# Performance work log

Hardware: AMD Instinct MI355X
Metric: run time of the kernel (lower is better)

## Reference

```python
import jax, jax.numpy as jnp
import numpy as np

N = 50000      # nodes
E = 800000     # edges (before self-loops)
IN_DIM = 128
HID = 64
OUT = 32
HEADS = 8
BN_EPS = 1e-5
NEG_SLOPE = 0.2  # PyG GATConv default


def setup_inputs() -> dict:
    key = jax.random.key(0)
    ks = jax.random.split(key, 24)
    g = lambda k, shape, fan_in: (jax.random.normal(k, shape, jnp.float32) / np.sqrt(fan_in))
    return {
        "x": jax.random.normal(ks[0], (N, IN_DIM), jnp.float32),
        "edge_index": jax.random.randint(ks[1], (2, E), 0, N, dtype=jnp.int64),
        # GCN1
        "gcn1_w": g(ks[2], (IN_DIM, HID), IN_DIM),
        "gcn1_b": jnp.zeros((HID,), jnp.float32),
        # BN1 (eval mode running stats)
        "bn1_gamma": jnp.ones((HID,), jnp.float32),
        "bn1_beta": jnp.zeros((HID,), jnp.float32),
        "bn1_mean": 0.1 * jax.random.normal(ks[3], (HID,), jnp.float32),
        "bn1_var": 0.5 + jax.random.uniform(ks[4], (HID,), jnp.float32),
        # GAT1: heads=8, per-head out=HID, concat=False -> mean over heads
        "gat1_w": g(ks[5], (HID, HEADS * HID), HID),
        "gat1_asrc": g(ks[6], (HEADS, HID), HID),
        "gat1_adst": g(ks[7], (HEADS, HID), HID),
        "gat1_b": jnp.zeros((HID,), jnp.float32),
        # GCN2
        "gcn2_w": g(ks[8], (HID, HID), HID),
        "gcn2_b": jnp.zeros((HID,), jnp.float32),
        # BN2
        "bn2_gamma": jnp.ones((HID,), jnp.float32),
        "bn2_beta": jnp.zeros((HID,), jnp.float32),
        "bn2_mean": 0.1 * jax.random.normal(ks[9], (HID,), jnp.float32),
        "bn2_var": 0.5 + jax.random.uniform(ks[10], (HID,), jnp.float32),
        # GAT2: heads=8, per-head out=OUT, concat=False
        "gat2_w": g(ks[11], (HID, HEADS * OUT), HID),
        "gat2_asrc": g(ks[12], (HEADS, OUT), OUT),
        "gat2_adst": g(ks[13], (HEADS, OUT), OUT),
        "gat2_b": jnp.zeros((OUT,), jnp.float32),
    }


def _gcn(x, src, dst, w, b, n):
    # PyG GCNConv: x @ W, symmetric norm with self-loops (src/dst already include them)
    h = x @ w
    deg = jax.ops.segment_sum(jnp.ones(src.shape[0], x.dtype), dst, num_segments=n)
    dinv = jnp.where(deg > 0, jax.lax.rsqrt(jnp.maximum(deg, 1.0)), 0.0)
    coef = dinv[src] * dinv[dst]                     # [E']
    out = jax.ops.segment_sum(coef[:, None] * h[src], dst, num_segments=n)
    return out + b


def _gat(x, src, dst, w, a_src, a_dst, b, n, heads, ch):
    # PyG GATConv (concat=False): mean over heads, softmax over incoming edges per dst
    h = (x @ w).reshape(n, heads, ch)                # [N,H,C]
    es = jnp.einsum('nhc,hc->nh', h, a_src)          # alpha_src per node
    ed = jnp.einsum('nhc,hc->nh', h, a_dst)
    e = jax.nn.leaky_relu(es[src] + ed[dst], NEG_SLOPE)  # [E',H]
    m = jax.ops.segment_max(e, dst, num_segments=n)
    m = jnp.where(jnp.isfinite(m), m, 0.0)
    ex = jnp.exp(e - m[dst])
    denom = jax.ops.segment_sum(ex, dst, num_segments=n)
    alpha = ex / (denom[dst] + 1e-16)                # [E',H]
    out = jnp.zeros((n, ch), x.dtype)
    for hd in range(heads):  # fixed small head loop keeps peak edge memory at [E',C]
        msg = alpha[:, hd, None] * h[src, hd]        # [E',C]
        out = out + jax.ops.segment_sum(msg, dst, num_segments=n)
    return out / heads + b


def _bn_eval(x, gamma, beta, mean, var):
    return (x - mean) * jax.lax.rsqrt(var + BN_EPS) * gamma + beta


def reference(x, edge_index,
              gcn1_w, gcn1_b, bn1_gamma, bn1_beta, bn1_mean, bn1_var,
              gat1_w, gat1_asrc, gat1_adst, gat1_b,
              gcn2_w, gcn2_b, bn2_gamma, bn2_beta, bn2_mean, bn2_var,
              gat2_w, gat2_asrc, gat2_adst, gat2_b):
    n = x.shape[0]
    loops = jnp.arange(n, dtype=edge_index.dtype)
    src = jnp.concatenate([edge_index[0], loops])    # self-loops (PyG default)
    dst = jnp.concatenate([edge_index[1], loops])

    h = _gcn(x, src, dst, gcn1_w, gcn1_b, n)
    h = jax.nn.relu(_bn_eval(h, bn1_gamma, bn1_beta, bn1_mean, bn1_var))
    h = jax.nn.relu(_gat(h, src, dst, gat1_w, gat1_asrc, gat1_adst, gat1_b, n, HEADS, HID))
    h = _gcn(h, src, dst, gcn2_w, gcn2_b, n)
    h = jax.nn.relu(_bn_eval(h, bn2_gamma, bn2_beta, bn2_mean, bn2_var))
    h = _gat(h, src, dst, gat2_w, gat2_asrc, gat2_adst, gat2_b, n, HEADS, OUT)
    return jax.nn.log_softmax(h, axis=1)
```

## Files before the change

kernel.cpp:

```cpp
#include <hip/hip_runtime.h>
#include <hip/hip_bf16.h>

#define NN 50000
#define NE 800000
#define IND 128
#define NH 8
#define EBLK 256
#define EPB 3125
#define NBUK 391
#define NBUKP 392
#define GH (NBUKP * EBLK)
#define PREPB 308

typedef __hip_bfloat16 bf16;
typedef __attribute__((ext_vector_type(8))) short short8;
typedef __attribute__((ext_vector_type(8))) __bf16 bf16x8;
typedef __attribute__((ext_vector_type(4))) float floatx4;
typedef __attribute__((ext_vector_type(2))) float floatx2;

static __device__ __forceinline__ short f2bf_bits(float f) {
    unsigned u = __float_as_uint(f);
    u = (u + 0x7fffu + ((u >> 16) & 1u)) >> 16;
    return (short)u;
}
static __device__ __forceinline__ float bf2f(bf16 v) { return __bfloat162float(v); }
static __device__ __forceinline__ floatx2 up2(unsigned av) {
    floatx2 r;
    r.x = __uint_as_float(av << 16);
    r.y = __uint_as_float(av & 0xffff0000u);
    return r;
}
static __device__ __forceinline__ unsigned pk2(float a, float b) {
    return (unsigned)(unsigned short)f2bf_bits(a) | ((unsigned)(unsigned short)f2bf_bits(b) << 16);
}
static __device__ __forceinline__ void pk_fma_lo(floatx2& acc, floatx2 a, floatx2 al) {
    asm("v_pk_fma_f32 %0, %1, %2, %0 op_sel:[0,0,0] op_sel_hi:[1,0,1]"
        : "+v"(acc) : "v"(a), "v"(al));
}
static __device__ __forceinline__ void pk_fma_hi(floatx2& acc, floatx2 a, floatx2 al) {
    asm("v_pk_fma_f32 %0, %1, %2, %0 op_sel:[0,1,0] op_sel_hi:[1,1,1]"
        : "+v"(acc) : "v"(a), "v"(al));
}

static __device__ __forceinline__ void scan_buckets(const int* __restrict__ bsum,
        int* sp, int* gb, int tid) {
    int v0 = (2 * tid < NBUKP) ? bsum[2 * tid] : 0;
    int v1 = (2 * tid + 1 < NBUKP) ? bsum[2 * tid + 1] : 0;
    int c = v0 + v1;
    sp[tid] = c; __syncthreads();
    int val = c;
#pragma unroll
    for (int off = 1; off < 256; off <<= 1) {
        int t = (tid >= off) ? sp[tid - off] : 0;
        __syncthreads();
        val += t; sp[tid] = val;
        __syncthreads();
    }
    int pex = val - c;
    gb[2 * tid] = pex;
    gb[2 * tid + 1] = pex + v0;
    __syncthreads();
}

__global__ __launch_bounds__(256) void bin_count_prep_kernel(const int* __restrict__ edst,
        int* __restrict__ ghist,
        const float* __restrict__ gcn1_w, const float* __restrict__ gcn2_w,
        const float* __restrict__ gat1_w, const float* __restrict__ gat2_w,
        const float* __restrict__ as1, const float* __restrict__ ad1,
        const float* __restrict__ as2, const float* __restrict__ ad2,
        bf16* __restrict__ wT1, bf16* __restrict__ wT2,
        bf16* __restrict__ wgT1, bf16* __restrict__ wgT2,
        float* __restrict__ was1, float* __restrict__ wad1,
        float* __restrict__ was2, float* __restrict__ wad2) {
    __shared__ int hsh[NBUKP];
    const int tid = threadIdx.x;
    if (blockIdx.x < EBLK) {
        const int blk = blockIdx.x;
        for (int b = tid; b < NBUKP; b += 256) hsh[b] = 0;
        __syncthreads();
        const int e0 = blk * EPB;
        for (int e = e0 + tid; e < e0 + EPB; e += 256)
            atomicAdd(&hsh[edst[e] >> 7], 1);
        __syncthreads();
        for (int b = tid; b < NBUKP; b += 256)
            ghist[b * EBLK + blk] = hsh[b];
    } else {
        int idx = (blockIdx.x - EBLK) * 256 + tid;
        if (idx < 8192) {
            int m = idx >> 7, k = idx & 127;
            ((short*)wT1)[idx] = f2bf_bits(gcn1_w[(long)k * 64 + m]);
        } else if (idx < 12288) {
            int i = idx - 8192;
            int m = i >> 6, k = i & 63;
            ((short*)wT2)[i] = f2bf_bits(gcn2_w[(long)k * 64 + m]);
        } else if (idx < 45056) {
            int i = idx - 12288;
            int m = i >> 9, k = i & 511;
            int h = k >> 6, c = k & 63;
            ((short*)wgT1)[i] = f2bf_bits(gat1_w[(long)c * 512 + h * 64 + m]);
        } else if (idx < 77824) {
            int i = idx - 45056;
            int m = i >> 9, k = i & 511;
            int h = k >> 6, c = k & 63;
            ((short*)wgT2)[i] = (m < 32) ? f2bf_bits(gat2_w[(long)c * 256 + h * 32 + m]) : (short)0;
        } else if (idx < 78336) {
            int i = idx - 77824;
            int h = i >> 6, c = i & 63;
            const float* wrow = gat1_w + (long)c * 512 + h * 64;
            float s = 0.f, d = 0.f;
            for (int cc = 0; cc < 64; ++cc) {
                float w = wrow[cc];
                s += w * as1[h * 64 + cc];
                d += w * ad1[h * 64 + cc];
            }
            was1[i] = s; wad1[i] = d;
        } else if (idx < 78848) {
            int i = idx - 78336;
            int h = i >> 6, c = i & 63;
            const float* wrow = gat2_w + (long)c * 256 + h * 32;
            float s = 0.f, d = 0.f;
            for (int cc = 0; cc < 32; ++cc) {
                float w = wrow[cc];
                s += w * as2[h * 32 + cc];
                d += w * ad2[h * 32 + cc];
            }
            was2[i] = s; wad2[i] = d;
        }
    }
}

__global__ __launch_bounds__(256) void scang1_kernel(const int* __restrict__ src,
        int* __restrict__ pre, int* __restrict__ bsum, int n) {
    __shared__ int sh[256];
    const int tid = threadIdx.x;
    const int idx = blockIdx.x * 256 + tid;
    int c = (idx < n) ? src[idx] : 0;
    sh[tid] = c; __syncthreads();
    int val = c;
#pragma unroll
    for (int off = 1; off < 256; off <<= 1) {
        int t = (tid >= off) ? sh[tid - off] : 0;
        __syncthreads();
        val += t; sh[tid] = val;
        __syncthreads();
    }
    if (idx < n) pre[idx] = val - c;
    if (tid == 255) bsum[blockIdx.x] = val;
}

__global__ __launch_bounds__(256) void bin_scatter_kernel(const int* __restrict__ esrc,
        const int* __restrict__ edst, const int* __restrict__ gpre,
        const int* __restrict__ bsum, unsigned* __restrict__ ebuf) {
    __shared__ int cur[NBUKP];
    __shared__ int sp[256], gb[512];
    const int tid = threadIdx.x, blk = blockIdx.x;
    scan_buckets(bsum, sp, gb, tid);
    for (int b = tid; b < NBUKP; b += 256)
        cur[b] = gpre[b * EBLK + blk] + gb[b];
    __syncthreads();
    const int e0 = blk * EPB;
    for (int e = e0 + tid; e < e0 + EPB; e += 256) {
        int d = edst[e], s = esrc[e];
        int pos = atomicAdd(&cur[d >> 7], 1);
        ebuf[pos] = ((unsigned)(d & 127) << 16) | (unsigned)s;
    }
}

__global__ __launch_bounds__(256) void bucket_finalize_kernel(const unsigned* __restrict__ ebuf,
        const int* __restrict__ gpre, const int* __restrict__ bsum,
        int* __restrict__ rowptr, float* __restrict__ dinv, int* __restrict__ csrc) {
    __shared__ int lh[128], lcur[128], sc[256];
    __shared__ int sp[256], gb[512];
    const int bu = blockIdx.x, tid = threadIdx.x;
    scan_buckets(bsum, sp, gb, tid);
    const int seg_beg = gpre[bu * EBLK] + gb[bu];
    const int seg_end = gpre[(bu + 1) * EBLK] + gb[bu + 1];
    if (tid < 128) lh[tid] = 0;
    __syncthreads();
    for (int i = seg_beg + tid; i < seg_end; i += 256)
        atomicAdd(&lh[ebuf[i] >> 16], 1);
    __syncthreads();
    int c = (tid < 128) ? lh[tid] : 0;
    sc[tid] = c; __syncthreads();
    int val = c;
#pragma unroll
    for (int off = 1; off < 256; off <<= 1) {
        int t = (tid >= off) ? sc[tid - off] : 0;
        __syncthreads();
        val += t; sc[tid] = val;
        __syncthreads();
    }
    int excl = val - c;
    if (tid < 128) {
        lcur[tid] = excl;
        int node = bu * 128 + tid;
        if (node < NN) {
            rowptr[node] = seg_beg + excl;
            dinv[node] = rsqrtf((float)c + 1.f);
        }
    }
    if (bu == 0 && tid == 0) rowptr[NN] = NE;
    __syncthreads();
    for (int i = seg_beg + tid; i < seg_end; i += 256) {
        unsigned u = ebuf[i];
        int pos = atomicAdd(&lcur[u >> 16], 1);
        csrc[seg_beg + pos] = (int)(u & 0xffffu);
    }
}

template<int K, int EPI, bool AF32>
__global__ __launch_bounds__(256) void mm2_kernel(const void* __restrict__ A,
        const bf16* __restrict__ wT, void* __restrict__ C,
        const float* __restrict__ bias, const float* __restrict__ rowscale,
        int nrows, int M) {
    const int row0 = blockIdx.x * 64;
    const int tid = threadIdx.x;
    const int lane = tid & 63, wave = tid >> 6;
    const int lr = lane & 15, q = lane >> 4;
    const int row = row0 + wave * 16 + lr;
    const bool rok = row < nrows;
    constexpr int NC = (EPI == 4) ? 2 : 4;
    floatx4 acc[NC] = {};
#pragma unroll 4
    for (int k0 = 0; k0 < K; k0 += 32) {
        short8 av = {0, 0, 0, 0, 0, 0, 0, 0};
        if (rok) {
            if (AF32) {
                const float* apf = (const float*)A + (long)row * K + q * 8 + k0;
                floatx4 va = *(const floatx4*)apf;
                floatx4 vb = *(const floatx4*)(apf + 4);
#pragma unroll
                for (int j = 0; j < 4; ++j) { av[j] = f2bf_bits(va[j]); av[4 + j] = f2bf_bits(vb[j]); }
            } else {
                av = *(const short8*)((const short*)A + (long)row * K + q * 8 + k0);
            }
        }
        bf16x8 a = __builtin_bit_cast(bf16x8, av);
#pragma unroll
        for (int c = 0; c < NC; ++c) {
            bf16x8 b = __builtin_bit_cast(bf16x8,
                *(const short8*)((const short*)wT + (long)(c * 16 + lr) * K + k0 + q * 8));
            acc[c] = __builtin_amdgcn_mfma_f32_16x16x32_bf16(a, b, acc[c], 0, 0, 0);
        }
    }
    if (EPI == 4) {
#pragma unroll
        for (int r = 0; r < 4; ++r) {
            int orow = row0 + wave * 16 + q * 4 + r;
            float v0 = acc[0][r] * 0.125f + bias[lr];
            float v1 = acc[1][r] * 0.125f + bias[16 + lr];
            float m = fmaxf(v0, v1);
#pragma unroll
            for (int off = 1; off < 16; off <<= 1) m = fmaxf(m, __shfl_xor(m, off));
            float s = __expf(v0 - m) + __expf(v1 - m);
#pragma unroll
            for (int off = 1; off < 16; off <<= 1) s += __shfl_xor(s, off);
            float ls = m + logf(s);
            if (orow < nrows) {
                ((float*)C)[(long)orow * 32 + lr] = v0 - ls;
                ((float*)C)[(long)orow * 32 + 16 + lr] = v1 - ls;
            }
        }
        return;
    }
#pragma unroll
    for (int c = 0; c < NC; ++c)
#pragma unroll
        for (int r = 0; r < 4; ++r) {
            int orow = row0 + wave * 16 + q * 4 + r;
            int col = c * 16 + lr;
            if (orow < nrows && col < M) {
                long o = (long)orow * M + col;
                float v = acc[c][r];
                if (EPI == 0) ((float*)C)[o] = v;
                else if (EPI == 2) {
                    v = v * 0.125f + bias[col];
                    ((bf16*)C)[o] = __float2bfloat16(fmaxf(v, 0.f));
                } else {
                    ((bf16*)C)[o] = __float2bfloat16(rowscale[orow] * v);
                }
            }
        }
}

__global__ __launch_bounds__(256) void gcn_fused_kernel(const int* __restrict__ rowptr,
        const int* __restrict__ csrc, const float* __restrict__ dinv,
        const bf16* __restrict__ hin, const float* __restrict__ b,
        const float* __restrict__ gamma, const float* __restrict__ beta,
        const float* __restrict__ mean, const float* __restrict__ var,
        bf16* __restrict__ actout) {
    const int node = blockIdx.x * 4 + (threadIdx.x >> 6);
    if (node >= NN) return;
    const int lane = threadIdx.x & 63;
    const int eslot = lane >> 5, cp = lane & 31;
    const unsigned cpo = 4u * (unsigned)cp;
    const int beg = __builtin_amdgcn_readfirstlane(rowptr[node]);
    const int end = __builtin_amdgcn_readfirstlane(rowptr[node + 1]);
    const float di = dinv[node];
    const int* csp = csrc + beg;
    floatx2 acc2 = {0.f, 0.f};
    const int dn = end - beg;
    const int kup = (dn + 15) & ~15;
    for (int k0 = 0; k0 < kup; k0 += 16) {
        int s_[8]; float w_[8];
#pragma unroll
        for (int u = 0; u < 8; ++u) {
            int k = k0 + 2 * u + eslot;
            int ok = k < dn;
            s_[u] = csp[ok ? k : 0];
            w_[u] = ok ? 1.f : 0.f;
        }
        unsigned av_[8];
#pragma unroll
        for (int u = 0; u < 8; ++u)
            av_[u] = *(const unsigned*)((const char*)hin + ((unsigned)s_[u] * 128u + cpo));
#pragma unroll
        for (int u = 0; u < 8; ++u) {
            floatx2 a2 = up2(av_[u]);
            acc2 += a2 * w_[u];
        }
    }
    acc2.x += __shfl_xor(acc2.x, 32);
    acc2.y += __shfl_xor(acc2.y, 32);
    {
        unsigned sv = *(const unsigned*)((const char*)hin + ((unsigned)node * 128u + cpo));
        acc2 += up2(sv);
    }
    int c0 = 2 * cp, c1 = c0 + 1;
    float x0 = acc2.x * di + b[c0];
    float x1 = acc2.y * di + b[c1];
    x0 = (x0 - mean[c0]) * rsqrtf(var[c0] + 1e-5f) * gamma[c0] + beta[c0];
    x1 = (x1 - mean[c1]) * rsqrtf(var[c1] + 1e-5f) * gamma[c1] + beta[c1];
    if (eslot == 0)
        *(unsigned*)((unsigned short*)actout + (long)node * 64 + c0) =
            pk2(fmaxf(x0, 0.f), fmaxf(x1, 0.f));
}

__global__ __launch_bounds__(256) void scores_kernel(const bf16* __restrict__ actb,
        const float* __restrict__ was, const float* __restrict__ wad,
        float* __restrict__ es, float* __restrict__ ed, int n) {
    const int node = blockIdx.x * 4 + (threadIdx.x >> 6);
    if (node >= n) return;
    const int lane = threadIdx.x & 63;
    const int h = lane >> 3, cg = lane & 7;
    short8 a8 = *(const short8*)((const short*)actb + (long)node * 64 + cg * 8);
    const float* wsp = was + h * 64 + cg * 8;
    const float* wdp = wad + h * 64 + cg * 8;
    floatx4 ws0 = *(const floatx4*)wsp, ws1 = *(const floatx4*)(wsp + 4);
    floatx4 wd0 = *(const floatx4*)wdp, wd1 = *(const floatx4*)(wdp + 4);
    float s = 0.f, d = 0.f;
#pragma unroll
    for (int j = 0; j < 4; ++j) {
        float v0 = bf2f(__builtin_bit_cast(bf16, a8[j]));
        float v1 = bf2f(__builtin_bit_cast(bf16, a8[4 + j]));
        s += v0 * ws0[j] + v1 * ws1[j];
        d += v0 * wd0[j] + v1 * wd1[j];
    }
#pragma unroll
    for (int off = 1; off < 8; off <<= 1) {
        s += __shfl_xor(s, off);
        d += __shfl_xor(d, off);
    }
    if (cg == 0) { es[node * NH + h] = s; ed[node * NH + h] = d; }
}

__global__ __launch_bounds__(256) void gat_agg_kernel(const int* __restrict__ rowptr,
        const int* __restrict__ csrc, const float* __restrict__ es, const float* __restrict__ ed,
        const bf16* __restrict__ actb, bf16* __restrict__ agg) {
    __shared__ __align__(16) float salpha[4][512];
    __shared__ int ssrcs[4][64];
    __shared__ __align__(16) float sself[4][8];
    const int wv = threadIdx.x >> 6;
    const int node = blockIdx.x * 4 + wv;
    if (node >= NN) return;
    const int lane = threadIdx.x & 63;
    const int h = lane & 7, slot = lane >> 3;
    const int beg = __builtin_amdgcn_readfirstlane(rowptr[node]);
    const int end = __builtin_amdgcn_readfirstlane(rowptr[node + 1]);
    const int deg = end - beg;
    const int* csp = csrc + beg;
    const float edr = *(const float*)((const char*)ed + ((unsigned)node * 32u + (unsigned)h * 4u));

    float selfe = *(const float*)((const char*)es + ((unsigned)node * 32u + (unsigned)h * 4u)) + edr;
    selfe = selfe > 0.f ? selfe : 0.2f * selfe;

    if (deg <= 64) {
        const int nb = (deg + 7) >> 3;
        const int dm1 = (deg > 0) ? deg - 1 : 0;
        float ex_r[8]; int s_r[8];
        float den = 0.f;
#pragma unroll
        for (int b = 0; b < 8; ++b) { ex_r[b] = 0.f; s_r[b] = 0; }
        if (deg > 0) {
#pragma unroll
            for (int b = 0; b < 8; ++b)
                if (b < nb) {
                    int k = b * 8 + slot;
                    s_r[b] = csp[k < deg ? k : dm1];
                }
#pragma unroll
            for (int b = 0; b < 8; ++b)
                if (b < nb) {
                    float e = *(const float*)((const char*)es +
                              ((unsigned)s_r[b] * 32u + (unsigned)h * 4u)) + edr;
                    e = e > 0.f ? e : 0.2f * e;
                    float ex = __expf(e - selfe);
                    ex_r[b] = (b * 8 + slot < deg) ? ex : 0.f;
                    den += ex_r[b];
                }
        }
        den += __shfl_xor(den, 8);
        den += __shfl_xor(den, 16);
        den += __shfl_xor(den, 32);
        const float invden = 1.f / (den + 1.f);

#pragma unroll
        for (int b = 0; b < 8; ++b)
            if (b < nb) salpha[wv][b * 64 + lane] = ex_r[b] * invden;
        if (h == 0) {
#pragma unroll
            for (int b = 0; b < 8; ++b)
                if (b < nb) ssrcs[wv][b * 8 + slot] = s_r[b];
        }
        if (slot == 0) sself[wv][h] = invden;

        const int hq = lane >> 5, cp = lane & 31;
        const unsigned cpo = 4u * (unsigned)cp;
        floatx2 acc2[4] = {};
        const int ng = nb;
        if (ng > 0) {
            int sA0, sA1, sA2, sA3, sA4, sA5, sA6, sA7;
            int sB0, sB1, sB2, sB3, sB4, sB5, sB6, sB7;
            unsigned rA0, rA1, rA2, rA3, rA4, rA5, rA6, rA7;
            unsigned rB0, rB1, rB2, rB3, rB4, rB5, rB6, rB7;
#define LOAD_BANK(S, R, G) do { \
    const int* sp_ = &ssrcs[wv][(G) * 8]; \
    S##0 = sp_[0]; S##1 = sp_[1]; S##2 = sp_[2]; S##3 = sp_[3]; \
    S##4 = sp_[4]; S##5 = sp_[5]; S##6 = sp_[6]; S##7 = sp_[7]; \
    R##0 = *(const unsigned*)((const char*)actb + ((unsigned)S##0 * 128u + cpo)); \
    R##1 = *(const unsigned*)((const char*)actb + ((unsigned)S##1 * 128u + cpo)); \
    R##2 = *(const unsigned*)((const char*)actb + ((unsigned)S##2 * 128u + cpo)); \
    R##3 = *(const unsigned*)((const char*)actb + ((unsigned)S##3 * 128u + cpo)); \
    R##4 = *(const unsigned*)((const char*)actb + ((unsigned)S##4 * 128u + cpo)); \
    R##5 = *(const unsigned*)((const char*)actb + ((unsigned)S##5 * 128u + cpo)); \
    R##6 = *(const unsigned*)((const char*)actb + ((unsigned)S##6 * 128u + cpo)); \
    R##7 = *(const unsigned*)((const char*)actb + ((unsigned)S##7 * 128u + cpo)); \
} while (0)
#define FMA_BANK(R, G) do { \
    const float* ab_ = &salpha[wv][(G) * 64 + hq * 4]; \
    unsigned rr_[8] = {R##0, R##1, R##2, R##3, R##4, R##5, R##6, R##7}; \
    _Pragma("unroll") \
    for (int j_ = 0; j_ < 8; ++j_) { \
        floatx4 al_ = *(const floatx4*)(ab_ + j_ * 8); \
        floatx2 al01_ = __builtin_shufflevector(al_, al_, 0, 1); \
        floatx2 al23_ = __builtin_shufflevector(al_, al_, 2, 3); \
        floatx2 a2_ = up2(rr_[j_]); \
        pk_fma_lo(acc2[0], a2_, al01_); pk_fma_hi(acc2[1], a2_, al01_); \
        pk_fma_lo(acc2[2], a2_, al23_); pk_fma_hi(acc2[3], a2_, al23_); \
    } \
} while (0)
            LOAD_BANK(sA, rA, 0);
            int g = 0;
            while (true) {
                if (g + 1 < ng) LOAD_BANK(sB, rB, g + 1);
                FMA_BANK(rA, g);
                ++g; if (g >= ng) break;
                if (g + 1 < ng) LOAD_BANK(sA, rA, g + 1);
                FMA_BANK(rB, g);
                ++g; if (g >= ng) break;
            }
#undef LOAD_BANK
#undef FMA_BANK
        }
        {
            unsigned sv = *(const unsigned*)((const char*)actb + ((unsigned)node * 128u + cpo));
            floatx2 a2 = up2(sv);
            floatx4 sa = *(const floatx4*)&sself[wv][hq * 4];
            floatx2 sa01 = __builtin_shufflevector(sa, sa, 0, 1);
            floatx2 sa23 = __builtin_shufflevector(sa, sa, 2, 3);
            pk_fma_lo(acc2[0], a2, sa01); pk_fma_hi(acc2[1], a2, sa01);
            pk_fma_lo(acc2[2], a2, sa23); pk_fma_hi(acc2[3], a2, sa23);
        }
#pragma unroll
        for (int j = 0; j < 4; ++j)
            *(unsigned*)((unsigned short*)agg + (long)node * 512 + (hq * 4 + j) * 64 + 2 * cp) =
                pk2(acc2[j].x, acc2[j].y);
    } else {
        float acc[NH] = {0.f, 0.f, 0.f, 0.f, 0.f, 0.f, 0.f, 0.f};
        float den = 0.f;
        for (int base = beg; base < end; base += 8) {
            int ei = base + slot;
            if (ei < end) {
                int s = csrc[ei];
                float e = es[s * NH + h] + edr;
                e = e > 0.f ? e : 0.2f * e;
                den += __expf(e - selfe);
            }
        }
        den += __shfl_xor(den, 8);
        den += __shfl_xor(den, 16);
        den += __shfl_xor(den, 32);
        const float invden = 1.f / (den + 1.f);
        for (int base = beg; base < end; base += 8) {
            int ei = base + slot;
            float al = 0.f; int sl = 0;
            if (ei < end) {
                sl = csrc[ei];
                float e = es[sl * NH + h] + edr;
                e = e > 0.f ? e : 0.2f * e;
                al = __expf(e - selfe) * invden;
            }
            salpha[wv][lane] = al;
            if (h == 0) ssrcs[wv][slot] = sl;
            int ecnt = end - base; if (ecnt > 8) ecnt = 8;
            for (int j = 0; j < ecnt; ++j) {
                int s = ssrcs[wv][j];
                float a = bf2f(actb[(long)s * 64 + lane]);
                floatx4 al0 = *(const floatx4*)&salpha[wv][j * 8];
                floatx4 al1 = *(const floatx4*)&salpha[wv][j * 8 + 4];
                acc[0] += al0[0] * a; acc[1] += al0[1] * a;
                acc[2] += al0[2] * a; acc[3] += al0[3] * a;
                acc[4] += al1[0] * a; acc[5] += al1[1] * a;
                acc[6] += al1[2] * a; acc[7] += al1[3] * a;
            }
        }
        {
            if (slot == 0) sself[wv][h] = invden;
            float a = bf2f(actb[(long)node * 64 + lane]);
            floatx4 s0 = *(const floatx4*)&sself[wv][0];
            floatx4 s1 = *(const floatx4*)&sself[wv][4];
            acc[0] += s0[0] * a; acc[1] += s0[1] * a;
            acc[2] += s0[2] * a; acc[3] += s0[3] * a;
            acc[4] += s1[0] * a; acc[5] += s1[1] * a;
            acc[6] += s1[2] * a; acc[7] += s1[3] * a;
        }
#pragma unroll
        for (int hh = 0; hh < NH; ++hh)
            agg[(long)node * 512 + hh * 64 + lane] = __float2bfloat16(acc[hh]);
    }
}

extern "C" void kernel_launch(void* const* d_in, const int* in_sizes, int n_in,
                              void* d_out, int out_size, void* d_ws, size_t ws_size,
                              hipStream_t stream) {
    const float* x        = (const float*)d_in[0];
    const int*   eidx     = (const int*)d_in[1];
    const float* gcn1_w   = (const float*)d_in[2];
    const float* gcn1_b   = (const float*)d_in[3];
    const float* bn1_g    = (const float*)d_in[4];
    const float* bn1_b    = (const float*)d_in[5];
    const float* bn1_m    = (const float*)d_in[6];
    const float* bn1_v    = (const float*)d_in[7];
    const float* gat1_w   = (const float*)d_in[8];
    const float* gat1_as  = (const float*)d_in[9];
    const float* gat1_ad  = (const float*)d_in[10];
    const float* gat1_b   = (const float*)d_in[11];
    const float* gcn2_w   = (const float*)d_in[12];
    const float* gcn2_b   = (const float*)d_in[13];
    const float* bn2_g    = (const float*)d_in[14];
    const float* bn2_b    = (const float*)d_in[15];
    const float* bn2_m    = (const float*)d_in[16];
    const float* bn2_v    = (const float*)d_in[17];
    const float* gat2_w   = (const float*)d_in[18];
    const float* gat2_as  = (const float*)d_in[19];
    const float* gat2_ad  = (const float*)d_in[20];
    const float* gat2_b   = (const float*)d_in[21];
    float* out = (float*)d_out;

    const int* esrc = eidx;
    const int* edst = eidx + NE;

    float* ws = (float*)d_ws;
    int*      ghist  = (int*)ws;
    int*      gpre   = ghist + GH;
    int*      gbsum  = gpre + GH;
    unsigned* ebuf   = (unsigned*)(gbsum + 512);
    int*      rowptr = (int*)(ebuf + NE);
    int*      csrc   = rowptr + 50048;
    float*    dinv   = (float*)(csrc + NE);
    float*    es     = dinv + 50048;
    float*    ed     = es + 400000;
    float*    was1   = ed + 400000;
    float*    wad1   = was1 + 512;
    float*    was2   = wad1 + 512;
    float*    wad2   = was2 + 512;
    bf16*     wT1    = (bf16*)(wad2 + 512);
    bf16*     wT2    = wT1 + 64 * 128;
    bf16*     wgT1   = wT2 + 64 * 64;
    bf16*     wgT2   = wgT1 + 64 * 512;
    bf16*     actb   = wgT2 + 64 * 512;
    bf16*     mmbf   = actb + (size_t)NN * 64;
    bf16*     agg    = mmbf + (size_t)NN * 64;

    auto cdiv = [](long a, long b) { return (int)((a + b - 1) / b); };
    const int GB = cdiv(NN, 64);
    const int NB = cdiv(NN, 4);

    bin_count_prep_kernel<<<EBLK + PREPB, 256, 0, stream>>>(edst, ghist,
        gcn1_w, gcn2_w, gat1_w, gat2_w, gat1_as, gat1_ad, gat2_as, gat2_ad,
        wT1, wT2, wgT1, wgT2, was1, wad1, was2, wad2);
    scang1_kernel<<<GH / 256, 256, 0, stream>>>(ghist, gpre, gbsum, GH);
    bin_scatter_kernel<<<EBLK, 256, 0, stream>>>(esrc, edst, gpre, gbsum, ebuf);
    bucket_finalize_kernel<<<NBUK, 256, 0, stream>>>(ebuf, gpre, gbsum, rowptr, dinv, csrc);

    mm2_kernel<IND, 3, true><<<GB, 256, 0, stream>>>(x, wT1, mmbf, nullptr, dinv, NN, 64);
    gcn_fused_kernel<<<NB, 256, 0, stream>>>(rowptr, csrc, dinv, mmbf,
        gcn1_b, bn1_g, bn1_b, bn1_m, bn1_v, actb);

    scores_kernel<<<NB, 256, 0, stream>>>(actb, was1, wad1, es, ed, NN);
    gat_agg_kernel<<<NB, 256, 0, stream>>>(rowptr, csrc, es, ed, actb, agg);
    mm2_kernel<512, 2, false><<<GB, 256, 0, stream>>>(agg, wgT1, actb, gat1_b, nullptr, NN, 64);

    mm2_kernel<64, 3, false><<<GB, 256, 0, stream>>>(actb, wT2, mmbf, nullptr, dinv, NN, 64);
    gcn_fused_kernel<<<NB, 256, 0, stream>>>(rowptr, csrc, dinv, mmbf,
        gcn2_b, bn2_g, bn2_b, bn2_m, bn2_v, actb);

    scores_kernel<<<NB, 256, 0, stream>>>(actb, was2, wad2, es, ed, NN);
    gat_agg_kernel<<<NB, 256, 0, stream>>>(rowptr, csrc, es, ed, actb, agg);
    mm2_kernel<512, 4, false><<<GB, 256, 0, stream>>>(agg, wgT2, out, gat2_b, nullptr, NN, 32);
}
```

Measured before the change: 364.0 us.

## Fuse GAT aggregation with head-projection GEMM and log-softmax epilogue

```diff
diff --git a/kernel.cpp b/kernel.cpp
--- a/kernel.cpp
+++ b/kernel.cpp
@@ -219,7 +219,7 @@
     const int lr = lane & 15, q = lane >> 4;
     const int row = row0 + wave * 16 + lr;
     const bool rok = row < nrows;
-    constexpr int NC = (EPI == 4) ? 2 : 4;
+    constexpr int NC = 4;
     floatx4 acc[NC] = {};
 #pragma unroll 4
     for (int k0 = 0; k0 < K; k0 += 32) {
@@ -242,26 +242,6 @@
                 *(const short8*)((const short*)wT + (long)(c * 16 + lr) * K + k0 + q * 8));
             acc[c] = __builtin_amdgcn_mfma_f32_16x16x32_bf16(a, b, acc[c], 0, 0, 0);
         }
-    }
-    if (EPI == 4) {
-#pragma unroll
-        for (int r = 0; r < 4; ++r) {
-            int orow = row0 + wave * 16 + q * 4 + r;
-            float v0 = acc[0][r] * 0.125f + bias[lr];
-            float v1 = acc[1][r] * 0.125f + bias[16 + lr];
-            float m = fmaxf(v0, v1);
-#pragma unroll
-            for (int off = 1; off < 16; off <<= 1) m = fmaxf(m, __shfl_xor(m, off));
-            float s = __expf(v0 - m) + __expf(v1 - m);
-#pragma unroll
-            for (int off = 1; off < 16; off <<= 1) s += __shfl_xor(s, off);
-            float ls = m + logf(s);
-            if (orow < nrows) {
-                ((float*)C)[(long)orow * 32 + lr] = v0 - ls;
-                ((float*)C)[(long)orow * 32 + 16 + lr] = v1 - ls;
-            }
-        }
-        return;
     }
 #pragma unroll
     for (int c = 0; c < NC; ++c)
@@ -364,79 +344,90 @@
     if (cg == 0) { es[node * NH + h] = s; ed[node * NH + h] = d; }
 }
 
-__global__ __launch_bounds__(256) void gat_agg_kernel(const int* __restrict__ rowptr,
+template<int NCT, int EPI>
+__global__ __launch_bounds__(256) void gat_fused_kernel(const int* __restrict__ rowptr,
         const int* __restrict__ csrc, const float* __restrict__ es, const float* __restrict__ ed,
-        const bf16* __restrict__ actb, bf16* __restrict__ agg) {
+        const bf16* __restrict__ actb, const bf16* __restrict__ wgT,
+        const float* __restrict__ bias, void* __restrict__ outp) {
     __shared__ __align__(16) float salpha[4][512];
     __shared__ int ssrcs[4][64];
     __shared__ __align__(16) float sself[4][8];
+    __shared__ __align__(16) unsigned short aggt[16][520];
+    __shared__ float redbuf[2][2][16];
     const int wv = threadIdx.x >> 6;
-    const int node = blockIdx.x * 4 + wv;
-    if (node >= NN) return;
     const int lane = threadIdx.x & 63;
     const int h = lane & 7, slot = lane >> 3;
-    const int beg = __builtin_amdgcn_readfirstlane(rowptr[node]);
-    const int end = __builtin_amdgcn_readfirstlane(rowptr[node + 1]);
-    const int deg = end - beg;
-    const int* csp = csrc + beg;
-    const float edr = *(const float*)((const char*)ed + ((unsigned)node * 32u + (unsigned)h * 4u));
-
-    float selfe = *(const float*)((const char*)es + ((unsigned)node * 32u + (unsigned)h * 4u)) + edr;
-    selfe = selfe > 0.f ? selfe : 0.2f * selfe;
-
-    if (deg <= 64) {
-        const int nb = (deg + 7) >> 3;
-        const int dm1 = (deg > 0) ? deg - 1 : 0;
-        float ex_r[8]; int s_r[8];
-        float den = 0.f;
-#pragma unroll
-        for (int b = 0; b < 8; ++b) { ex_r[b] = 0.f; s_r[b] = 0; }
-        if (deg > 0) {
+    const int hq = lane >> 5, cp = lane & 31;
+    const unsigned cpo = 4u * (unsigned)cp;
+
+#pragma unroll 1
+    for (int nn = 0; nn < 4; ++nn) {
+        const int row = wv * 4 + nn;
+        const int node = blockIdx.x * 16 + row;
+        const int beg = __builtin_amdgcn_readfirstlane(rowptr[node]);
+        const int end = __builtin_amdgcn_readfirstlane(rowptr[node + 1]);
+        const int deg = end - beg;
+        const int* csp = csrc + beg;
+        const float edr = *(const float*)((const char*)ed + ((unsigned)node * 32u + (unsigned)h * 4u));
+        float selfe = *(const float*)((const char*)es + ((unsigned)node * 32u + (unsigned)h * 4u)) + edr;
+        selfe = selfe > 0.f ? selfe : 0.2f * selfe;
+
+        if (deg <= 64) {
+            const int nb = (deg + 7) >> 3;
+            const int dm1 = (deg > 0) ? deg - 1 : 0;
+            float ex_r[8]; int s_r[8];
+            float den = 0.f;
+#pragma unroll
+            for (int b = 0; b < 8; ++b) { ex_r[b] = 0.f; s_r[b] = 0; }
+            if (deg > 0) {
+#pragma unroll
+                for (int b = 0; b < 8; ++b)
+                    if (b < nb) {
+                        int k = b * 8 + slot;
+                        s_r[b] = csp[k < deg ? k : dm1];
+                    }
+#pragma unroll
+                for (int b = 0; b < 8; ++b)
+                    if (b < nb) {
+                        float e = *(const float*)((const char*)es +
+                                  ((unsigned)s_r[b] * 32u + (unsigned)h * 4u)) + edr;
+                        e = e > 0.f ? e : 0.2f * e;
+                        float ex = __expf(e - selfe);
+                        ex_r[b] = (b * 8 + slot < deg) ? ex : 0.f;
+                        den += ex_r[b];
+                    }
+            }
+            den += __shfl_xor(den, 8);
+            den += __shfl_xor(den, 16);
+            den += __shfl_xor(den, 32);
+            const float invden = 1.f / (den + 1.f);
 #pragma unroll
             for (int b = 0; b < 8; ++b)
-                if (b < nb) {
-                    int k = b * 8 + slot;
-                    s_r[b] = csp[k < deg ? k : dm1];
-                }
-#pragma unroll
-            for (int b = 0; b < 8; ++b)
-                if (b < nb) {
-                    float e = *(const float*)((const char*)es +
-                              ((unsigned)s_r[b] * 32u + (unsigned)h * 4u)) + edr;
-                    e = e > 0.f ? e : 0.2f * e;
-                    float ex = __expf(e - selfe);
-                    ex_r[b] = (b * 8 + slot < deg) ? ex : 0.f;
-                    den += ex_r[b];
-                }
-        }
-        den += __shfl_xor(den, 8);
-        den += __shfl_xor(den, 16);
-        den += __shfl_xor(den, 32);
-        const float invden = 1.f / (den + 1.f);
-
-#pragma unroll
-        for (int b = 0; b < 8; ++b)
-            if (b < nb) salpha[wv][b * 64 + lane] = ex_r[b] * invden;
-        if (h == 0) {
-#pragma unroll
-            for (int b = 0; b < 8; ++b)
-                if (b < nb) ssrcs[wv][b * 8 + slot] = s_r[b];
-        }
-        if (slot == 0) sself[wv][h] = invden;
-
-        const int hq = lane >> 5, cp = lane & 31;
-        const unsigned cpo = 4u * (unsigned)cp;
-        floatx2 acc2[4] = {};
-        const int ng = nb;
-        if (ng > 0) {
-            int sA0, sA1, sA2, sA3, sA4, sA5, sA6, sA7;
-            int sB0, sB1, sB2, sB3, sB4, sB5, sB6, sB7;
-            unsigned rA0, rA1, rA2, rA3, rA4, rA5, rA6, rA7;
-            unsigned rB0, rB1, rB2, rB3, rB4, rB5, rB6, rB7;
+                if (b < nb) salpha[wv][b * 64 + lane] = ex_r[b] * invden;
+            if (h == 0) {
+#pragma unroll
+                for (int b = 0; b < 8; ++b)
+                    if (b < nb) ssrcs[wv][b * 8 + slot] = s_r[b];
+            }
+            if (slot == 0) sself[wv][h] = invden;
+
+            floatx2 acc2[4] = {};
+            const int ng = nb;
+            if (ng > 0) {
+                int sA0, sA1, sA2, sA3, sA4, sA5, sA6, sA7;
+                int sB0, sB1, sB2, sB3, sB4, sB5, sB6, sB7;
+                unsigned rA0, rA1, rA2, rA3, rA4, rA5, rA6, rA7;
+                unsigned rB0, rB1, rB2, rB3, rB4, rB5, rB6, rB7;
 #define LOAD_BANK(S, R, G) do { \
     const int* sp_ = &ssrcs[wv][(G) * 8]; \
-    S##0 = sp_[0]; S##1 = sp_[1]; S##2 = sp_[2]; S##3 = sp_[3]; \
-    S##4 = sp_[4]; S##5 = sp_[5]; S##6 = sp_[6]; S##7 = sp_[7]; \
+    S##0 = __builtin_amdgcn_readfirstlane(sp_[0]); \
+    S##1 = __builtin_amdgcn_readfirstlane(sp_[1]); \
+    S##2 = __builtin_amdgcn_readfirstlane(sp_[2]); \
+    S##3 = __builtin_amdgcn_readfirstlane(sp_[3]); \
+    S##4 = __builtin_amdgcn_readfirstlane(sp_[4]); \
+    S##5 = __builtin_amdgcn_readfirstlane(sp_[5]); \
+    S##6 = __builtin_amdgcn_readfirstlane(sp_[6]); \
+    S##7 = __builtin_amdgcn_readfirstlane(sp_[7]); \
     R##0 = *(const unsigned*)((const char*)actb + ((unsigned)S##0 * 128u + cpo)); \
     R##1 = *(const unsigned*)((const char*)actb + ((unsigned)S##1 * 128u + cpo)); \
     R##2 = *(const unsigned*)((const char*)actb + ((unsigned)S##2 * 128u + cpo)); \
@@ -459,84 +450,155 @@
         pk_fma_lo(acc2[2], a2_, al23_); pk_fma_hi(acc2[3], a2_, al23_); \
     } \
 } while (0)
-            LOAD_BANK(sA, rA, 0);
-            int g = 0;
-            while (true) {
-                if (g + 1 < ng) LOAD_BANK(sB, rB, g + 1);
-                FMA_BANK(rA, g);
-                ++g; if (g >= ng) break;
-                if (g + 1 < ng) LOAD_BANK(sA, rA, g + 1);
-                FMA_BANK(rB, g);
-                ++g; if (g >= ng) break;
-            }
+                LOAD_BANK(sA, rA, 0);
+                int g = 0;
+                while (true) {
+                    if (g + 1 < ng) LOAD_BANK(sB, rB, g + 1);
+                    __builtin_amdgcn_sched_barrier(0);
+                    FMA_BANK(rA, g);
+                    ++g; if (g >= ng) break;
+                    if (g + 1 < ng) LOAD_BANK(sA, rA, g + 1);
+                    __builtin_amdgcn_sched_barrier(0);
+                    FMA_BANK(rB, g);
+                    ++g; if (g >= ng) break;
+                }
 #undef LOAD_BANK
 #undef FMA_BANK
-        }
-        {
-            unsigned sv = *(const unsigned*)((const char*)actb + ((unsigned)node * 128u + cpo));
-            floatx2 a2 = up2(sv);
-            floatx4 sa = *(const floatx4*)&sself[wv][hq * 4];
-            floatx2 sa01 = __builtin_shufflevector(sa, sa, 0, 1);
-            floatx2 sa23 = __builtin_shufflevector(sa, sa, 2, 3);
-            pk_fma_lo(acc2[0], a2, sa01); pk_fma_hi(acc2[1], a2, sa01);
-            pk_fma_lo(acc2[2], a2, sa23); pk_fma_hi(acc2[3], a2, sa23);
-        }
-#pragma unroll
-        for (int j = 0; j < 4; ++j)
-            *(unsigned*)((unsigned short*)agg + (long)node * 512 + (hq * 4 + j) * 64 + 2 * cp) =
-                pk2(acc2[j].x, acc2[j].y);
+            }
+            {
+                unsigned sv = *(const unsigned*)((const char*)actb + ((unsigned)node * 128u + cpo));
+                floatx2 a2 = up2(sv);
+                floatx4 sa = *(const floatx4*)&sself[wv][hq * 4];
+                floatx2 sa01 = __builtin_shufflevector(sa, sa, 0, 1);
+                floatx2 sa23 = __builtin_shufflevector(sa, sa, 2, 3);
+                pk_fma_lo(acc2[0], a2, sa01); pk_fma_hi(acc2[1], a2, sa01);
+                pk_fma_lo(acc2[2], a2, sa23); pk_fma_hi(acc2[3], a2, sa23);
+            }
+#pragma unroll
+            for (int j = 0; j < 4; ++j)
+                *(unsigned*)&aggt[row][(hq * 4 + j) * 64 + 2 * cp] = pk2(acc2[j].x, acc2[j].y);
+        } else {
+            float acc[NH] = {0.f, 0.f, 0.f, 0.f, 0.f, 0.f, 0.f, 0.f};
+            float den = 0.f;
+            for (int base = beg; base < end; base += 8) {
+                int ei = base + slot;
+                if (ei < end) {
+                    int s = csrc[ei];
+                    float e = es[s * NH + h] + edr;
+                    e = e > 0.f ? e : 0.2f * e;
+                    den += __expf(e - selfe);
+                }
+            }
+            den += __shfl_xor(den, 8);
+            den += __shfl_xor(den, 16);
+            den += __shfl_xor(den, 32);
+            const float invden = 1.f / (den + 1.f);
+            for (int base = beg; base < end; base += 8) {
+                int ei = base + slot;
+                float al = 0.f; int sl = 0;
+                if (ei < end) {
+                    sl = csrc[ei];
+                    float e = es[sl * NH + h] + edr;
+                    e = e > 0.f ? e : 0.2f * e;
+                    al = __expf(e - selfe) * invden;
+                }
+                salpha[wv][lane] = al;
+                if (h == 0) ssrcs[wv][slot] = sl;
+                int ecnt = end - base; if (ecnt > 8) ecnt = 8;
+                for (int j = 0; j < ecnt; ++j) {
+                    int s = ssrcs[wv][j];
+                    float a = bf2f(actb[(long)s * 64 + lane]);
+                    floatx4 al0 = *(const floatx4*)&salpha[wv][j * 8];
+                    floatx4 al1 = *(const floatx4*)&salpha[wv][j * 8 + 4];
+                    acc[0] += al0[0] * a; acc[1] += al0[1] * a;
+                    acc[2] += al0[2] * a; acc[3] += al0[3] * a;
+                    acc[4] += al1[0] * a; acc[5] += al1[1] * a;
+                    acc[6] += al1[2] * a; acc[7] += al1[3] * a;
+                }
+            }
+            {
+                if (slot == 0) sself[wv][h] = invden;
+                float a = bf2f(actb[(long)node * 64 + lane]);
+                floatx4 s0 = *(const floatx4*)&sself[wv][0];
+                floatx4 s1 = *(const floatx4*)&sself[wv][4];
+                acc[0] += s0[0] * a; acc[1] += s0[1] * a;
+                acc[2] += s0[2] * a; acc[3] += s0[3] * a;
+                acc[4] += s1[0] * a; acc[5] += s1[1] * a;
+                acc[6] += s1[2] * a; acc[7] += s1[3] * a;
+            }
+#pragma unroll
+            for (int hh = 0; hh < NH; ++hh)
+                aggt[row][hh * 64 + lane] = (unsigned short)f2bf_bits(acc[hh]);
+        }
+    }
+
+    __syncthreads();
+
+    const int lr = lane & 15, q = lane >> 4;
+    const bool act = wv < NCT;
+    floatx4 acc = {};
+    if (act) {
+#pragma unroll 4
+        for (int k0 = 0; k0 < 512; k0 += 32) {
+            bf16x8 a = __builtin_bit_cast(bf16x8,
+                *(const short8*)&aggt[lr][k0 + q * 8]);
+            bf16x8 b = __builtin_bit_cast(bf16x8,
+                *(const short8*)((const short*)wgT + (long)(wv * 16 + lr) * 512 + k0 + q * 8));
+            acc = __builtin_amdgcn_mfma_f32_16x16x32_bf16(a, b, acc, 0, 0, 0);
+        }
+    }
+
+    if (EPI == 2) {
+        if (act) {
+#pragma unroll
+            for (int r = 0; r < 4; ++r) {
+                int node = blockIdx.x * 16 + q * 4 + r;
+                int col = wv * 16 + lr;
+                float v = acc[r] * 0.125f + bias[col];
+                ((bf16*)outp)[(long)node * 64 + col] = __float2bfloat16(fmaxf(v, 0.f));
+            }
+        }
     } else {
-        float acc[NH] = {0.f, 0.f, 0.f, 0.f, 0.f, 0.f, 0.f, 0.f};
-        float den = 0.f;
-        for (int base = beg; base < end; base += 8) {
-            int ei = base + slot;
-            if (ei < end) {
-                int s = csrc[ei];
-                float e = es[s * NH + h] + edr;
-                e = e > 0.f ? e : 0.2f * e;
-                den += __expf(e - selfe);
-            }
-        }
-        den += __shfl_xor(den, 8);
-        den += __shfl_xor(den, 16);
-        den += __shfl_xor(den, 32);
-        const float invden = 1.f / (den + 1.f);
-        for (int base = beg; base < end; base += 8) {
-            int ei = base + slot;
-            float al = 0.f; int sl = 0;
-            if (ei < end) {
-                sl = csrc[ei];
-                float e = es[sl * NH + h] + edr;
-                e = e > 0.f ? e : 0.2f * e;
-                al = __expf(e - selfe) * invden;
-            }
-            salpha[wv][lane] = al;
-            if (h == 0) ssrcs[wv][slot] = sl;
-            int ecnt = end - base; if (ecnt > 8) ecnt = 8;
-            for (int j = 0; j < ecnt; ++j) {
-                int s = ssrcs[wv][j];
-                float a = bf2f(actb[(long)s * 64 + lane]);
-                floatx4 al0 = *(const floatx4*)&salpha[wv][j * 8];
-                floatx4 al1 = *(const floatx4*)&salpha[wv][j * 8 + 4];
-                acc[0] += al0[0] * a; acc[1] += al0[1] * a;
-                acc[2] += al0[2] * a; acc[3] += al0[3] * a;
-                acc[4] += al1[0] * a; acc[5] += al1[1] * a;
-                acc[6] += al1[2] * a; acc[7] += al1[3] * a;
-            }
-        }
-        {
-            if (slot == 0) sself[wv][h] = invden;
-            float a = bf2f(actb[(long)node * 64 + lane]);
-            floatx4 s0 = *(const floatx4*)&sself[wv][0];
-            floatx4 s1 = *(const floatx4*)&sself[wv][4];
-            acc[0] += s0[0] * a; acc[1] += s0[1] * a;
-            acc[2] += s0[2] * a; acc[3] += s0[3] * a;
-            acc[4] += s1[0] * a; acc[5] += s1[1] * a;
-            acc[6] += s1[2] * a; acc[7] += s1[3] * a;
-        }
-#pragma unroll
-        for (int hh = 0; hh < NH; ++hh)
-            agg[(long)node * 512 + hh * 64 + lane] = __float2bfloat16(acc[hh]);
+        float v[4], m[4];
+#pragma unroll
+        for (int r = 0; r < 4; ++r) {
+            v[r] = acc[r] * 0.125f + (act ? bias[wv * 16 + lr] : 0.f);
+            m[r] = v[r];
+        }
+#pragma unroll
+        for (int off = 1; off < 16; off <<= 1)
+#pragma unroll
+            for (int r = 0; r < 4; ++r) m[r] = fmaxf(m[r], __shfl_xor(m[r], off));
+        if (act && lr == 0) {
+#pragma unroll
+            for (int r = 0; r < 4; ++r) redbuf[0][wv][q * 4 + r] = m[r];
+        }
+        __syncthreads();
+        float s[4];
+#pragma unroll
+        for (int r = 0; r < 4; ++r) {
+            float mm_ = fmaxf(redbuf[0][0][q * 4 + r], redbuf[0][1][q * 4 + r]);
+            m[r] = mm_;
+            s[r] = act ? __expf(v[r] - mm_) : 0.f;
+        }
+#pragma unroll
+        for (int off = 1; off < 16; off <<= 1)
+#pragma unroll
+            for (int r = 0; r < 4; ++r) s[r] += __shfl_xor(s[r], off);
+        if (act && lr == 0) {
+#pragma unroll
+            for (int r = 0; r < 4; ++r) redbuf[1][wv][q * 4 + r] = s[r];
+        }
+        __syncthreads();
+        if (act) {
+#pragma unroll
+            for (int r = 0; r < 4; ++r) {
+                int row = q * 4 + r;
+                int node = blockIdx.x * 16 + row;
+                float ls = m[r] + logf(redbuf[1][0][row] + redbuf[1][1][row]);
+                ((float*)outp)[(long)node * 32 + wv * 16 + lr] = v[r] - ls;
+            }
+        }
     }
 }
 
@@ -590,11 +652,12 @@
     bf16*     wgT2   = wgT1 + 64 * 512;
     bf16*     actb   = wgT2 + 64 * 512;
     bf16*     mmbf   = actb + (size_t)NN * 64;
-    bf16*     agg    = mmbf + (size_t)NN * 64;
+    bf16*     gact   = mmbf + (size_t)NN * 64;
 
     auto cdiv = [](long a, long b) { return (int)((a + b - 1) / b); };
     const int GB = cdiv(NN, 64);
     const int NB = cdiv(NN, 4);
+    const int FB = NN / 16;
 
     bin_count_prep_kernel<<<EBLK + PREPB, 256, 0, stream>>>(edst, ghist,
         gcn1_w, gcn2_w, gat1_w, gat2_w, gat1_as, gat1_ad, gat2_as, gat2_ad,
@@ -608,14 +671,12 @@
         gcn1_b, bn1_g, bn1_b, bn1_m, bn1_v, actb);
 
     scores_kernel<<<NB, 256, 0, stream>>>(actb, was1, wad1, es, ed, NN);
-    gat_agg_kernel<<<NB, 256, 0, stream>>>(rowptr, csrc, es, ed, actb, agg);
-    mm2_kernel<512, 2, false><<<GB, 256, 0, stream>>>(agg, wgT1, actb, gat1_b, nullptr, NN, 64);
-
-    mm2_kernel<64, 3, false><<<GB, 256, 0, stream>>>(actb, wT2, mmbf, nullptr, dinv, NN, 64);
+    gat_fused_kernel<4, 2><<<FB, 256, 0, stream>>>(rowptr, csrc, es, ed, actb, wgT1, gat1_b, gact);
+
+    mm2_kernel<64, 3, false><<<GB, 256, 0, stream>>>(gact, wT2, mmbf, nullptr, dinv, NN, 64);
     gcn_fused_kernel<<<NB, 256, 0, stream>>>(rowptr, csrc, dinv, mmbf,
         gcn2_b, bn2_g, bn2_b, bn2_m, bn2_v, actb);
 
     scores_kernel<<<NB, 256, 0, stream>>>(actb, was2, wad2, es, ed, NN);
-    gat_agg_kernel<<<NB, 256, 0, stream>>>(rowptr, csrc, es, ed, actb, agg);
-    mm2_kernel<512, 4, false><<<GB, 256, 0, stream>>>(agg, wgT2, out, gat2_b, nullptr, NN, 32);
-}
+    gat_fused_kernel<2, 4><<<FB, 256, 0, stream>>>(rowptr, csrc, es, ed, actb, wgT2, gat2_b, out);
+}
```

Measured after the change: 347.6 us. 4.5% less time.
